# Kernel optimization log

Measured on AMD Instinct MI355X. Metric: run time of the kernel, lower is better.

The kernel has to match this reference:

```python
import jax, jax.numpy as jnp
import numpy as np

L_LAYERS, D, H, V, S, B = 12, 1024, 16, 50257, 512, 4
DH = D // H
DFF = 4 * D
EPS = 1e-6
STD = 0.02


def setup_inputs() -> dict:
    key = jax.random.key(0)
    ks = jax.random.split(key, 16)
    n = lambda k, shp: (jax.random.normal(k, shp, dtype=jnp.float32) * STD)
    inp = {
        'in_idx': jax.random.randint(ks[0], (B, S), 0, V, dtype=jnp.int32),
        'tok_emb': n(ks[1], (V, D)),          # tied with out_head
        'pos_emb': n(ks[2], (S, D)),
        # per-layer stacked params; Linear stored as [in, out] so y = x @ W
        'Wq': n(ks[3], (L_LAYERS, D, D)),
        'Wk': n(ks[4], (L_LAYERS, D, D)),
        'Wv': n(ks[5], (L_LAYERS, D, D)),
        'Wo': n(ks[6], (L_LAYERS, D, D)),
        'bo': jnp.zeros((L_LAYERS, D), jnp.float32),
        'W1': n(ks[7], (L_LAYERS, D, DFF)),
        'b1': jnp.zeros((L_LAYERS, DFF), jnp.float32),
        'W2': n(ks[8], (L_LAYERS, DFF, D)),
        'b2': jnp.zeros((L_LAYERS, D), jnp.float32),
        'ln1_s': jnp.ones((L_LAYERS, D), jnp.float32),
        'ln1_b': jnp.zeros((L_LAYERS, D), jnp.float32),
        'ln2_s': jnp.ones((L_LAYERS, D), jnp.float32),
        'ln2_b': jnp.zeros((L_LAYERS, D), jnp.float32),
        'lnf_s': jnp.ones((D,), jnp.float32),
        'lnf_b': jnp.zeros((D,), jnp.float32),
    }
    return inp


def _layernorm(x, scale, shift):
    mean = jnp.mean(x, axis=-1, keepdims=True)
    var = jnp.mean(jnp.square(x - mean), axis=-1, keepdims=True)  # unbiased=False
    return scale * (x - mean) / jnp.sqrt(var + EPS) + shift


def _gelu(x):
    c = jnp.sqrt(jnp.asarray(2.0 / jnp.pi, x.dtype))
    return 0.5 * x * (1.0 + jnp.tanh(c * (x + 0.044715 * x * x * x)))


def _gpt_forward(in_idx, tok_emb, pos_emb, Wq, Wk, Wv, Wo, bo, W1, b1, W2, b2,
                 ln1_s, ln1_b, ln2_s, ln2_b, lnf_s, lnf_b):
    b, s = in_idx.shape
    x = tok_emb[in_idx] + pos_emb[:s]  # [B,S,D]
    causal = jnp.triu(jnp.ones((s, s), bool), k=1)  # True above diagonal
    scale = 1.0 / jnp.sqrt(jnp.asarray(DH, x.dtype))
    for i in range(L_LAYERS):
        # --- attention sublayer ---
        h = _layernorm(x, ln1_s[i], ln1_b[i])
        q = (h @ Wq[i]).reshape(b, s, H, DH)
        k = (h @ Wk[i]).reshape(b, s, H, DH)
        v = (h @ Wv[i]).reshape(b, s, H, DH)
        scores = jnp.einsum('bqhd,bkhd->bhqk', q, k)
        scores = jnp.where(causal, -jnp.inf, scores) * scale
        attn = jax.nn.softmax(scores, axis=-1)
        ctx = jnp.einsum('bhqk,bkhd->bqhd', attn, v).reshape(b, s, D)
        x = x + ctx @ Wo[i] + bo[i]
        # --- feed-forward sublayer ---
        h = _layernorm(x, ln2_s[i], ln2_b[i])
        x = x + _gelu(h @ W1[i] + b1[i]) @ W2[i] + b2[i]
    x = _layernorm(x, lnf_s, lnf_b)
    logits = x @ tok_emb.T  # tied out head (no bias)
    return logits


def reference(in_idx, tok_emb, pos_emb, Wq, Wk, Wv, Wo, bo, W1, b1, W2, b2,
              ln1_s, ln1_b, ln2_s, ln2_b, lnf_s, lnf_b):
    return _gpt_forward(in_idx, tok_emb, pos_emb, Wq, Wk, Wv, Wo, bo, W1, b1,
                        W2, b2, ln1_s, ln1_b, ln2_s, ln2_b, lnf_s, lnf_b)
```

## Files before the change

### kernel.cpp

```cpp
#include <hip/hip_runtime.h>


#define LL 12
#define DM 1024
#define NH 16
#define DHD 64
#define NV 50257
#define NVP 50432
#define SQ 512
#define NB 4
#define DF 4096
#define MR (NB * SQ)

typedef short bf16x8 __attribute__((ext_vector_type(8)));
typedef float f32x4 __attribute__((ext_vector_type(4)));
typedef unsigned short u16;

__device__ __forceinline__ u16 f2b(float f) {
  unsigned u = __float_as_uint(f);
  u += 0x7fff + ((u >> 16) & 1);
  return (u16)(u >> 16);
}

__device__ __forceinline__ void gload16(const u16* g, u16* l) {
  __builtin_amdgcn_global_load_lds(
      (const __attribute__((address_space(1))) unsigned*)g,
      (__attribute__((address_space(3))) unsigned*)l, 16, 0, 0);
}

template <int MODE, int TBM, int TBN, int MTLOG>
__global__ __launch_bounds__(256, 2) void gemm_k(
    const u16* __restrict__ A, const u16* __restrict__ B, void* __restrict__ Cp,
    void* __restrict__ Cp2, void* __restrict__ Cp3,
    const float* __restrict__ bias, int N, int K, int lda, int ldb, int ldc) {
  int id = blockIdx.x;
  int q8 = gridDim.x >> 3;
  int swz = (id & 7) * q8 + (id >> 3);
  int mt = swz & ((1 << MTLOG) - 1), nt = swz >> MTLOG;
  int m0 = mt * TBM, n0 = nt * TBN;

  __shared__ u16 As[2][TBM * 64];
  __shared__ u16 Bs[2][TBN * 64];

  int t = threadIdx.x, lane = t & 63, wave = t >> 6;
  int wm = wave >> 1, wn = wave & 1;
  int lr = lane & 15, g = lane >> 4;
  int srow = lane >> 3;
  int sxcol = ((lane & 7) ^ (lane >> 3)) << 3;
  int rsw = (lr & 7) << 3;
  constexpr int FM = TBM / 32, FN = TBN / 32;
  constexpr int CA = TBM / 32, CB = TBN / 32;

  f32x4 acc[FM][FN];
#pragma unroll
  for (int i = 0; i < FM; ++i)
#pragma unroll
    for (int j = 0; j < FN; ++j) acc[i][j] = (f32x4){0.f, 0.f, 0.f, 0.f};

  auto stage = [&](int buf, int kt) {
    int k0 = kt * 64;
#pragma unroll
    for (int v = 0; v < CA; ++v) {
      int c = v * 4 + wave;
      gload16(A + (size_t)(m0 + c * 8 + srow) * lda + k0 + sxcol,
              &As[buf][c * 512]);
    }
#pragma unroll
    for (int v = 0; v < CB; ++v) {
      int c = v * 4 + wave;
      gload16(B + (size_t)(n0 + c * 8 + srow) * ldb + k0 + sxcol,
              &Bs[buf][c * 512]);
    }
  };

  auto compute = [&](int buf) {
    bf16x8 af[FM][2], bq[FN][2];
#pragma unroll
    for (int ks = 0; ks < 2; ++ks) {
      int co = (ks * 32 + g * 8) ^ rsw;
#pragma unroll
      for (int i = 0; i < FM; ++i)
        af[i][ks] =
            *(const bf16x8*)&As[buf][(wm * (TBM / 2) + i * 16 + lr) * 64 + co];
#pragma unroll
      for (int j = 0; j < FN; ++j)
        bq[j][ks] =
            *(const bf16x8*)&Bs[buf][(wn * (TBN / 2) + j * 16 + lr) * 64 + co];
    }
#pragma unroll
    for (int ks = 0; ks < 2; ++ks)
#pragma unroll
      for (int i = 0; i < FM; ++i)
#pragma unroll
        for (int j = 0; j < FN; ++j)
          acc[i][j] = __builtin_amdgcn_mfma_f32_16x16x32_bf16(
              af[i][ks], bq[j][ks], acc[i][j], 0, 0, 0);
  };

  int nk = K >> 6;
  stage(0, 0);
  __syncthreads();
  int cur = 0;
  for (int kt = 0; kt < nk - 1; ++kt) {
    stage(cur ^ 1, kt + 1);
    compute(cur);
    __syncthreads();
    cur ^= 1;
  }
  compute(cur);

  int rb = g * 4;
#pragma unroll
  for (int i = 0; i < FM; ++i) {
#pragma unroll
    for (int j = 0; j < FN; ++j) {
      int m = m0 + wm * (TBM / 2) + i * 16 + rb;
      int n = n0 + wn * (TBN / 2) + j * 16 + lr;
      f32x4 a = acc[i][j];
      if constexpr (MODE == 1) {
        float* C = (float*)Cp;
        float bv = bias[n];
#pragma unroll
        for (int r = 0; r < 4; ++r) {
          size_t ix = (size_t)(m + r) * ldc + n;
          C[ix] += a[r] + bv;
        }
      } else if constexpr (MODE == 2) {
        u16* C = (u16*)Cp;
        float bv = bias[n];
#pragma unroll
        for (int r = 0; r < 4; ++r) {
          float u2 = a[r] + bv;
          float gl =
              0.5f * u2 *
              (1.f + tanhf(0.7978845608f * (u2 + 0.044715f * u2 * u2 * u2)));
          C[(size_t)(m + r) * ldc + n] = f2b(gl);
        }
      } else if constexpr (MODE == 7) {
        int sel = n >> 10, nn = n & 1023;
        if (sel < 2) {
          u16* C = sel == 0 ? (u16*)Cp : (u16*)Cp2;
#pragma unroll
          for (int r = 0; r < 4; ++r) C[(size_t)(m + r) * ldc + nn] = f2b(a[r]);
        } else {
          u16* C = (u16*)Cp3;
          int bb = m >> 9, s2 = m & (SQ - 1);
          ushort4 w4;
          w4.x = f2b(a[0]); w4.y = f2b(a[1]);
          w4.z = f2b(a[2]); w4.w = f2b(a[3]);
          *(ushort4*)&C[((size_t)bb * DM + nn) * SQ + s2] = w4;
        }
      }
    }
  }
}

__global__ __launch_bounds__(512, 2) void gemmL_k(const u16* __restrict__ A,
                                                  const u16* __restrict__ B,
                                                  float* __restrict__ C) {
  int id = blockIdx.x;
  int q8 = gridDim.x >> 3;
  int swz = (id & 7) * q8 + (id >> 3);
  int mt = swz & 7, nt = swz >> 3;
  int m0 = mt * 256, n0 = nt * 256;

  __shared__ u16 As[2][256 * 64];
  __shared__ u16 Bs[2][256 * 64];

  int t = threadIdx.x, lane = t & 63, wave = t >> 6;
  int wm = wave >> 2, wn = wave & 3;
  int lr = lane & 15, g = lane >> 4;
  int rsw = (lr & 7) << 3;

  f32x4 acc[8][4];
#pragma unroll
  for (int i = 0; i < 8; ++i)
#pragma unroll
    for (int j = 0; j < 4; ++j) acc[i][j] = (f32x4){0.f, 0.f, 0.f, 0.f};

  auto stage = [&](int slot, int kt) {
    int k0 = kt * 64;
#pragma unroll
    for (int v = 0; v < 4; ++v) {
      int c = v * 512 + t;
      int row = c >> 3, cc = c & 7;
      gload16(A + (size_t)(m0 + row) * DM + k0 + ((cc ^ (row & 7)) << 3),
              &As[slot][c * 8]);
    }
#pragma unroll
    for (int v = 0; v < 4; ++v) {
      int c = v * 512 + t;
      int row = c >> 3, cc = c & 7;
      gload16(B + (size_t)(n0 + row) * DM + k0 + ((cc ^ (row & 7)) << 3),
              &Bs[slot][c * 8]);
    }
  };

  auto phase = [&](int slot, int ks) {
    int co = (ks * 32 + g * 8) ^ rsw;
    bf16x8 af[8], bq[4];
#pragma unroll
    for (int i = 0; i < 8; ++i)
      af[i] = *(const bf16x8*)&As[slot][(wm * 128 + i * 16 + lr) * 64 + co];
#pragma unroll
    for (int j = 0; j < 4; ++j)
      bq[j] = *(const bf16x8*)&Bs[slot][(wn * 64 + j * 16 + lr) * 64 + co];
    __builtin_amdgcn_s_setprio(1);
#pragma unroll
    for (int i = 0; i < 8; ++i)
#pragma unroll
      for (int j = 0; j < 4; ++j)
        acc[i][j] = __builtin_amdgcn_mfma_f32_16x16x32_bf16(af[i], bq[j],
                                                            acc[i][j], 0, 0, 0);
    __builtin_amdgcn_s_setprio(0);
  };

  constexpr int NIT = DM / 128;
  stage(0, 0);
  stage(1, 1);
#pragma unroll 1
  for (int it = 0; it < NIT; ++it) {
    asm volatile("s_waitcnt vmcnt(8)" ::: "memory");
    __builtin_amdgcn_s_barrier();
    phase(0, 0);
    phase(0, 1);
    __builtin_amdgcn_s_barrier();
    if (it + 1 < NIT) {
      stage(0, 2 * it + 2);
      asm volatile("s_waitcnt vmcnt(8)" ::: "memory");
    } else {
      asm volatile("s_waitcnt vmcnt(0)" ::: "memory");
    }
    __builtin_amdgcn_s_barrier();
    phase(1, 0);
    phase(1, 1);
    __builtin_amdgcn_s_barrier();
    if (it + 1 < NIT) stage(1, 2 * it + 3);
  }

  int rb = g * 4;
#pragma unroll
  for (int i = 0; i < 8; ++i) {
#pragma unroll
    for (int j = 0; j < 4; ++j) {
      int m = m0 + wm * 128 + i * 16 + rb;
      int n = n0 + wn * 64 + j * 16 + lr;
      if (n < NV) {
        f32x4 a = acc[i][j];
#pragma unroll
        for (int r = 0; r < 4; ++r) C[(size_t)(m + r) * NV + n] = a[r];
      }
    }
  }
}

__global__ __launch_bounds__(256) void fattn_k(const u16* __restrict__ qb,
                                               const u16* __restrict__ kb,
                                               const u16* __restrict__ vt,
                                               u16* __restrict__ cx) {
  int id = blockIdx.x;
  int qt = id >> 6, bh = id & 63;
  int b = bh >> 4, hh = bh & 15;
  int t = threadIdx.x, lane = t & 63, w = t >> 6;
  int lr = lane & 15, g = lane >> 4;

  __shared__ u16 Kt[64 * 72];
  __shared__ u16 Vt[64 * 72];
  __shared__ u16 Pl[4 * 16 * 72];

  int qw = qt * 64 + w * 16;

  bf16x8 aQ[2];
#pragma unroll
  for (int f = 0; f < 2; ++f)
    aQ[f] = *(const bf16x8*)&qb[(size_t)(b * SQ + qw + lr) * DM + hh * DHD +
                                f * 32 + g * 8];

  f32x4 o[4];
#pragma unroll
  for (int j = 0; j < 4; ++j) o[j] = (f32x4){0.f, 0.f, 0.f, 0.f};
  f32x4 m4 = (f32x4){-3e38f, -3e38f, -3e38f, -3e38f};
  f32x4 l4 = (f32x4){0.f, 0.f, 0.f, 0.f};
  u16* Pw = &Pl[w * 16 * 72];

  for (int kt = 0; kt <= qt; ++kt) {
    int k0 = kt * 64;
#pragma unroll
    for (int it = 0; it < 2; ++it) {
      int c = t + it * 256;
      int row = c >> 3, ch = c & 7;
      int4 kv = *(const int4*)&kb[(size_t)(b * SQ + k0 + row) * DM + hh * DHD +
                                  ch * 8];
      int4 vv = *(const int4*)&vt[(size_t)(b * DM + hh * DHD + row) * SQ + k0 +
                                  ch * 8];
      *(int4*)&Kt[row * 72 + ch * 8] = kv;
      *(int4*)&Vt[row * 72 + ch * 8] = vv;
    }
    __syncthreads();

    f32x4 s[4];
#pragma unroll
    for (int j = 0; j < 4; ++j) s[j] = (f32x4){0.f, 0.f, 0.f, 0.f};
#pragma unroll
    for (int j = 0; j < 4; ++j)
#pragma unroll
      for (int f = 0; f < 2; ++f) {
        bf16x8 bk = *(const bf16x8*)&Kt[(j * 16 + lr) * 72 + f * 32 + g * 8];
        s[j] =
            __builtin_amdgcn_mfma_f32_16x16x32_bf16(aQ[f], bk, s[j], 0, 0, 0);
      }
#pragma unroll
    for (int j = 0; j < 4; ++j) {
      int kcol = k0 + j * 16 + lr;
#pragma unroll
      for (int r = 0; r < 4; ++r) {
        float sv = s[j][r] * 0.125f;
        if (kt == qt && kcol > qw + g * 4 + r) sv = -1e30f;
        s[j][r] = sv;
      }
    }
    f32x4 fr;
#pragma unroll
    for (int r = 0; r < 4; ++r) {
      float v = fmaxf(fmaxf(s[0][r], s[1][r]), fmaxf(s[2][r], s[3][r]));
#pragma unroll
      for (int d = 1; d < 16; d <<= 1) v = fmaxf(v, __shfl_xor(v, d));
      float mn = fmaxf(m4[r], v);
      fr[r] = __expf(m4[r] - mn);
      m4[r] = mn;
    }
#pragma unroll
    for (int j = 0; j < 4; ++j)
#pragma unroll
      for (int r = 0; r < 4; ++r) o[j][r] *= fr[r];
    f32x4 ps = (f32x4){0.f, 0.f, 0.f, 0.f};
#pragma unroll
    for (int j = 0; j < 4; ++j)
#pragma unroll
      for (int r = 0; r < 4; ++r) {
        float p = __expf(s[j][r] - m4[r]);
        s[j][r] = p;
        ps[r] += p;
      }
#pragma unroll
    for (int r = 0; r < 4; ++r) {
      float v = ps[r];
#pragma unroll
      for (int d = 1; d < 16; d <<= 1) v += __shfl_xor(v, d);
      l4[r] = l4[r] * fr[r] + v;
    }
#pragma unroll
    for (int j = 0; j < 4; ++j)
#pragma unroll
      for (int r = 0; r < 4; ++r)
        Pw[(g * 4 + r) * 72 + j * 16 + lr] = f2b(s[j][r]);
#pragma unroll
    for (int f = 0; f < 2; ++f) {
      bf16x8 ap = *(const bf16x8*)&Pw[lr * 72 + f * 32 + g * 8];
#pragma unroll
      for (int j = 0; j < 4; ++j) {
        bf16x8 bv = *(const bf16x8*)&Vt[(j * 16 + lr) * 72 + f * 32 + g * 8];
        o[j] = __builtin_amdgcn_mfma_f32_16x16x32_bf16(ap, bv, o[j], 0, 0, 0);
      }
    }
    __syncthreads();
  }

#pragma unroll
  for (int r = 0; r < 4; ++r) {
    float inv = 1.f / l4[r];
#pragma unroll
    for (int j = 0; j < 4; ++j)
      cx[(size_t)(b * SQ + qw + g * 4 + r) * DM + hh * DHD + j * 16 + lr] =
          f2b(o[j][r] * inv);
  }
}

__global__ __launch_bounds__(256) void transpln_k(
    const float* __restrict__ Wq, const float* __restrict__ Wk,
    const float* __restrict__ Wv, const float* __restrict__ Wo,
    const float* __restrict__ W1, const float* __restrict__ W2,
    u16* __restrict__ wb, const float* __restrict__ x,
    const float* __restrict__ sc, const float* __restrict__ sh,
    u16* __restrict__ o) {
  __shared__ u16 tl[64][72];
  __shared__ float red[8];
  int t = threadIdx.x;
  if (blockIdx.x < 3072) {
    int id = blockIdx.x;
    const float* src;
    u16* dst;
    int K, N, ktile, ntile;
    if (id < 1024) {
      int mat = id >> 8, rem = id & 255;
      ntile = rem & 15; ktile = rem >> 4;
      src = mat == 0 ? Wq : mat == 1 ? Wk : mat == 2 ? Wv : Wo;
      dst = wb + (size_t)mat * DM * DM;
      K = DM; N = DM;
    } else if (id < 2048) {
      int rem = id - 1024;
      ntile = rem & 63; ktile = rem >> 6;
      src = W1; dst = wb + (size_t)4 * DM * DM;
      K = DM; N = DF;
    } else {
      int rem = id - 2048;
      ntile = rem & 15; ktile = rem >> 4;
      src = W2; dst = wb + (size_t)4 * DM * DM + (size_t)DM * DF;
      K = DF; N = DM;
    }
    int n0 = ntile * 64, k0 = ktile * 64;
    int tn = (t & 15) * 4, tk = t >> 4;
#pragma unroll
    for (int it = 0; it < 4; ++it) {
      int k = tk + it * 16;
      float4 v = *(const float4*)(src + (size_t)(k0 + k) * N + n0 + tn);
      tl[tn + 0][k] = f2b(v.x);
      tl[tn + 1][k] = f2b(v.y);
      tl[tn + 2][k] = f2b(v.z);
      tl[tn + 3][k] = f2b(v.w);
    }
    __syncthreads();
    int wn = t >> 3, wk = (t & 7) * 8;
#pragma unroll
    for (int it = 0; it < 2; ++it) {
      int n = wn + it * 32;
      int4 v = *(const int4*)&tl[n][wk];
      *(int4*)(dst + (size_t)(n0 + n) * K + k0 + wk) = v;
    }
  } else {
    int row = blockIdx.x - 3072;
    const float* xr = x + (size_t)row * DM;
    float4 v = *(const float4*)(xr + t * 4);
    float s = v.x + v.y + v.z + v.w;
#pragma unroll
    for (int d = 32; d; d >>= 1) s += __shfl_xor(s, d);
    if ((t & 63) == 0) red[t >> 6] = s;
    __syncthreads();
    float mean = (red[0] + red[1] + red[2] + red[3]) * (1.f / DM);
    float dx = v.x - mean, dy = v.y - mean, dz = v.z - mean, dw = v.w - mean;
    float s2 = dx * dx + dy * dy + dz * dz + dw * dw;
#pragma unroll
    for (int d = 32; d; d >>= 1) s2 += __shfl_xor(s2, d);
    if ((t & 63) == 0) red[4 + (t >> 6)] = s2;
    __syncthreads();
    float var = (red[4] + red[5] + red[6] + red[7]) * (1.f / DM);
    float rstd = 1.f / sqrtf(var + 1e-6f);
    float4 gg = *(const float4*)(sc + t * 4);
    float4 b = *(const float4*)(sh + t * 4);
    ushort4 w4;
    w4.x = f2b(gg.x * (dx * rstd) + b.x);
    w4.y = f2b(gg.y * (dy * rstd) + b.y);
    w4.z = f2b(gg.z * (dz * rstd) + b.z);
    w4.w = f2b(gg.w * (dw * rstd) + b.w);
    *(ushort4*)(o + (size_t)row * DM + t * 4) = w4;
  }
}

__global__ __launch_bounds__(256) void ln_k(const float* __restrict__ x,
                                            const float* __restrict__ sc,
                                            const float* __restrict__ sh,
                                            u16* __restrict__ o) {
  int row = blockIdx.x, t = threadIdx.x;
  const float* xr = x + (size_t)row * DM;
  float4 v = *(const float4*)(xr + t * 4);
  float s = v.x + v.y + v.z + v.w;
#pragma unroll
  for (int d = 32; d; d >>= 1) s += __shfl_xor(s, d);
  __shared__ float red[8];
  if ((t & 63) == 0) red[t >> 6] = s;
  __syncthreads();
  float mean = (red[0] + red[1] + red[2] + red[3]) * (1.f / DM);
  float dx = v.x - mean, dy = v.y - mean, dz = v.z - mean, dw = v.w - mean;
  float s2 = dx * dx + dy * dy + dz * dz + dw * dw;
#pragma unroll
  for (int d = 32; d; d >>= 1) s2 += __shfl_xor(s2, d);
  if ((t & 63) == 0) red[4 + (t >> 6)] = s2;
  __syncthreads();
  float var = (red[4] + red[5] + red[6] + red[7]) * (1.f / DM);
  float rstd = 1.f / sqrtf(var + 1e-6f);
  float4 g = *(const float4*)(sc + t * 4);
  float4 b = *(const float4*)(sh + t * 4);
  ushort4 w4;
  w4.x = f2b(g.x * (dx * rstd) + b.x);
  w4.y = f2b(g.y * (dy * rstd) + b.y);
  w4.z = f2b(g.z * (dz * rstd) + b.z);
  w4.w = f2b(g.w * (dw * rstd) + b.w);
  *(ushort4*)(o + (size_t)row * DM + t * 4) = w4;
}

__global__ __launch_bounds__(256) void embtok_k(const int* __restrict__ idx,
                                                const float* __restrict__ tok,
                                                const float* __restrict__ pos,
                                                float* __restrict__ x,
                                                u16* __restrict__ tokT) {
  int t = threadIdx.x;
  if (blockIdx.x < MR) {
    int row = blockIdx.x;
    int s = row & (SQ - 1);
    int id = idx[row];
    float4 a = *(const float4*)(tok + (size_t)id * DM + t * 4);
    float4 p = *(const float4*)(pos + (size_t)s * DM + t * 4);
    a.x += p.x; a.y += p.y; a.z += p.z; a.w += p.w;
    *(float4*)(x + (size_t)row * DM + t * 4) = a;
  } else {
    size_t r = blockIdx.x - MR;
    ushort4 w = {0, 0, 0, 0};
    if (r < NV) {
      float4 v = *(const float4*)(tok + r * DM + t * 4);
      w.x = f2b(v.x); w.y = f2b(v.y); w.z = f2b(v.z); w.w = f2b(v.w);
    }
    *(ushort4*)(tokT + r * DM + t * 4) = w;
  }
}

extern "C" void kernel_launch(void* const* d_in, const int* in_sizes, int n_in,
                              void* d_out, int out_size, void* d_ws,
                              size_t ws_size, hipStream_t stream) {
  const int* idx = (const int*)d_in[0];
  const float* tok = (const float*)d_in[1];
  const float* pos = (const float*)d_in[2];
  const float* Wq = (const float*)d_in[3];
  const float* Wk = (const float*)d_in[4];
  const float* Wv = (const float*)d_in[5];
  const float* Wo = (const float*)d_in[6];
  const float* bo = (const float*)d_in[7];
  const float* W1 = (const float*)d_in[8];
  const float* b1 = (const float*)d_in[9];
  const float* W2 = (const float*)d_in[10];
  const float* b2 = (const float*)d_in[11];
  const float* ln1s = (const float*)d_in[12];
  const float* ln1b = (const float*)d_in[13];
  const float* ln2s = (const float*)d_in[14];
  const float* ln2b = (const float*)d_in[15];
  const float* lnfs = (const float*)d_in[16];
  const float* lnfb = (const float*)d_in[17];
  float* out = (float*)d_out;

  char* w = (char*)d_ws;
  float* x = (float*)w;  w += (size_t)MR * DM * 4;
  u16* h = (u16*)w;      w += (size_t)MR * DM * 2;
  u16* qb = (u16*)w;     w += (size_t)MR * DM * 2;
  u16* kb = (u16*)w;     w += (size_t)MR * DM * 2;
  u16* vt = (u16*)w;     w += (size_t)NB * DM * SQ * 2;
  u16* ff = (u16*)w;     w += (size_t)MR * DF * 2;
  u16* wb = (u16*)w;     w += ((size_t)4 * DM * DM + 2 * (size_t)DM * DF) * 2;
  u16* tokT = (u16*)w;
  u16* cx = h;
  u16* wo_b = wb + (size_t)3 * DM * DM;
  u16* wb1 = wb + (size_t)4 * DM * DM;
  u16* wb2 = wb1 + (size_t)DM * DF;

  dim3 T(256);
  embtok_k<<<MR + NVP, T, 0, stream>>>(idx, tok, pos, x, tokT);
  for (int l = 0; l < LL; ++l) {
    size_t wo_ = (size_t)l * DM * DM;
    size_t w1_ = (size_t)l * DM * DF;
    transpln_k<<<5120, T, 0, stream>>>(Wq + wo_, Wk + wo_, Wv + wo_, Wo + wo_,
                                       W1 + w1_, W2 + w1_, wb, x, ln1s + l * DM,
                                       ln1b + l * DM, h);
    gemm_k<7, 64, 128, 5><<<768, T, 0, stream>>>(
        h, wb, qb, kb, vt, nullptr, 3 * DM, DM, DM, DM, DM);
    fattn_k<<<512, T, 0, stream>>>(qb, kb, vt, cx);
    gemm_k<1, 64, 64, 5><<<512, T, 0, stream>>>(
        cx, wo_b, x, nullptr, nullptr, bo + l * DM, DM, DM, DM, DM, DM);
    ln_k<<<MR, T, 0, stream>>>(x, ln2s + l * DM, ln2b + l * DM, h);
    gemm_k<2, 128, 128, 4><<<512, T, 0, stream>>>(
        h, wb1, ff, nullptr, nullptr, b1 + l * DF, DF, DM, DM, DM, DF);
    gemm_k<1, 64, 64, 5><<<512, T, 0, stream>>>(
        ff, wb2, x, nullptr, nullptr, b2 + l * DM, DM, DF, DF, DF, DM);
  }
  ln_k<<<MR, T, 0, stream>>>(x, lnfs, lnfb, h);
  gemmL_k<<<1576, dim3(512), 0, stream>>>(h, tokT, out);
}
```

Before: 2.435 ms.

## Deepen logits GEMM prefetch with triple-buffered B tiles and decoupled A/B staging

Restructures the output-head GEMM pipeline so A and B tiles are staged separately. B gets a third LDS buffer, so B is prefetched three k-tiles ahead and A two. The loop now runs one barrier pair per 64-wide k-tile, with sched_barriers to keep the compiler from reordering loads across compute. Launch bounds drop to one block per CU, which matches the larger LDS footprint and gives more register headroom. The cost is more LDS, less room for overlapping blocks, and hand-counted vmcnt waits that must match the issue order exactly.

```diff
diff --git a/kernel.cpp b/kernel.cpp
--- a/kernel.cpp
+++ b/kernel.cpp
@@ -155,7 +155,7 @@
   }
 }
 
-__global__ __launch_bounds__(512, 2) void gemmL_k(const u16* __restrict__ A,
+__global__ __launch_bounds__(512, 1) void gemmL_k(const u16* __restrict__ A,
                                                   const u16* __restrict__ B,
                                                   float* __restrict__ C) {
   int id = blockIdx.x;
@@ -165,7 +165,7 @@
   int m0 = mt * 256, n0 = nt * 256;
 
   __shared__ u16 As[2][256 * 64];
-  __shared__ u16 Bs[2][256 * 64];
+  __shared__ u16 Bs[3][256 * 64];
 
   int t = threadIdx.x, lane = t & 63, wave = t >> 6;
   int wm = wave >> 2, wn = wave & 3;
@@ -178,7 +178,7 @@
 #pragma unroll
     for (int j = 0; j < 4; ++j) acc[i][j] = (f32x4){0.f, 0.f, 0.f, 0.f};
 
-  auto stage = [&](int slot, int kt) {
+  auto stageA = [&](int slot, int kt) {
     int k0 = kt * 64;
 #pragma unroll
     for (int v = 0; v < 4; ++v) {
@@ -187,6 +187,9 @@
       gload16(A + (size_t)(m0 + row) * DM + k0 + ((cc ^ (row & 7)) << 3),
               &As[slot][c * 8]);
     }
+  };
+  auto stageB = [&](int slot, int kt) {
+    int k0 = kt * 64;
 #pragma unroll
     for (int v = 0; v < 4; ++v) {
       int c = v * 512 + t;
@@ -195,48 +198,52 @@
               &Bs[slot][c * 8]);
     }
   };
-
-  auto phase = [&](int slot, int ks) {
-    int co = (ks * 32 + g * 8) ^ rsw;
-    bf16x8 af[8], bq[4];
-#pragma unroll
-    for (int i = 0; i < 8; ++i)
-      af[i] = *(const bf16x8*)&As[slot][(wm * 128 + i * 16 + lr) * 64 + co];
-#pragma unroll
-    for (int j = 0; j < 4; ++j)
-      bq[j] = *(const bf16x8*)&Bs[slot][(wn * 64 + j * 16 + lr) * 64 + co];
-    __builtin_amdgcn_s_setprio(1);
-#pragma unroll
-    for (int i = 0; i < 8; ++i)
+  auto compute = [&](int sa, int sb) {
+#pragma unroll
+    for (int ks = 0; ks < 2; ++ks) {
+      int co = (ks * 32 + g * 8) ^ rsw;
+      bf16x8 af[8], bq[4];
+#pragma unroll
+      for (int i = 0; i < 8; ++i)
+        af[i] = *(const bf16x8*)&As[sa][(wm * 128 + i * 16 + lr) * 64 + co];
 #pragma unroll
       for (int j = 0; j < 4; ++j)
-        acc[i][j] = __builtin_amdgcn_mfma_f32_16x16x32_bf16(af[i], bq[j],
-                                                            acc[i][j], 0, 0, 0);
-    __builtin_amdgcn_s_setprio(0);
+        bq[j] = *(const bf16x8*)&Bs[sb][(wn * 64 + j * 16 + lr) * 64 + co];
+      __builtin_amdgcn_s_setprio(1);
+#pragma unroll
+      for (int i = 0; i < 8; ++i)
+#pragma unroll
+        for (int j = 0; j < 4; ++j)
+          acc[i][j] = __builtin_amdgcn_mfma_f32_16x16x32_bf16(
+              af[i], bq[j], acc[i][j], 0, 0, 0);
+      __builtin_amdgcn_s_setprio(0);
+    }
   };
 
-  constexpr int NIT = DM / 128;
-  stage(0, 0);
-  stage(1, 1);
+  stageB(0, 0); stageA(0, 0); stageB(1, 1); stageA(1, 1); stageB(2, 2);
+  int sb = 0;
 #pragma unroll 1
-  for (int it = 0; it < NIT; ++it) {
-    asm volatile("s_waitcnt vmcnt(8)" ::: "memory");
+  for (int kt = 0; kt < 14; ++kt) {
+    asm volatile("s_waitcnt vmcnt(12)" ::: "memory");
     __builtin_amdgcn_s_barrier();
-    phase(0, 0);
-    phase(0, 1);
+    __builtin_amdgcn_sched_barrier(0);
+    compute(kt & 1, sb);
     __builtin_amdgcn_s_barrier();
-    if (it + 1 < NIT) {
-      stage(0, 2 * it + 2);
-      asm volatile("s_waitcnt vmcnt(8)" ::: "memory");
-    } else {
-      asm volatile("s_waitcnt vmcnt(0)" ::: "memory");
-    }
-    __builtin_amdgcn_s_barrier();
-    phase(1, 0);
-    phase(1, 1);
-    __builtin_amdgcn_s_barrier();
-    if (it + 1 < NIT) stage(1, 2 * it + 3);
-  }
+    __builtin_amdgcn_sched_barrier(0);
+    stageA(kt & 1, kt + 2);
+    if (kt < 13) stageB(sb, kt + 3);
+    sb = sb + 1 == 3 ? 0 : sb + 1;
+  }
+  asm volatile("s_waitcnt vmcnt(8)" ::: "memory");
+  __builtin_amdgcn_s_barrier();
+  __builtin_amdgcn_sched_barrier(0);
+  compute(0, 2);
+  __builtin_amdgcn_s_barrier();
+  __builtin_amdgcn_sched_barrier(0);
+  asm volatile("s_waitcnt vmcnt(0)" ::: "memory");
+  __builtin_amdgcn_s_barrier();
+  __builtin_amdgcn_sched_barrier(0);
+  compute(1, 0);
 
   int rb = g * 4;
 #pragma unroll
```

Measured after the change: 2.248 ms. -7.7%, faster.
